# Kernel optimization log

Hardware: AMD Instinct MI355X
Metric: run time of the kernel (lower is better)

## Reference

```python
import jax, jax.numpy as jnp
import numpy as np

B, L, D_MODEL, H = 2, 2048, 1024, 16
D_HEAD = D_MODEL // H
NEG = -1e9


def setup_inputs() -> dict:
    key = jax.random.key(0)
    ks = jax.random.split(key, 8)
    q = jax.random.normal(ks[0], (B, L, D_MODEL), dtype=jnp.float32)
    k = jax.random.normal(ks[1], (B, L, D_MODEL), dtype=jnp.float32)
    v = jax.random.normal(ks[2], (B, L, D_MODEL), dtype=jnp.float32)
    # causal mask: True where attention is disallowed (masked_fill semantics)
    mask = jnp.broadcast_to(jnp.triu(jnp.ones((L, L), dtype=bool), k=1), (B, L, L))
    s = 1.0 / np.sqrt(D_MODEL)
    Wq = jax.random.normal(ks[3], (D_MODEL, D_MODEL), dtype=jnp.float32) * s
    Wk = jax.random.normal(ks[4], (D_MODEL, D_MODEL), dtype=jnp.float32) * s
    Wv = jax.random.normal(ks[5], (D_MODEL, D_MODEL), dtype=jnp.float32) * s
    Wo = jax.random.normal(ks[6], (D_MODEL, D_MODEL), dtype=jnp.float32) * s
    return {"q": q, "k": k, "v": v, "mask": mask,
            "Wq": Wq, "Wk": Wk, "Wv": Wv, "Wo": Wo}


def reference(q, k, v, mask, Wq, Wk, Wv, Wo):
    # projections (Linear, bias=False)
    qh = (q @ Wq).reshape(B, L, H, D_HEAD)
    kh = (k @ Wk).reshape(B, L, H, D_HEAD)
    vh = (v @ Wv).reshape(B, L, H, D_HEAD)
    # per-head scores: contiguous d_model slices == head reshape
    scores = jnp.einsum("bqhd,bkhd->bhqk", qh, kh)
    scores = jnp.where(mask[:, None, :, :], NEG, scores)
    # NOTE: original applies softmax FIRST, then divides by sqrt(d_head)
    weights = jax.nn.softmax(scores, axis=-1) / np.sqrt(D_HEAD).astype(np.float32)
    att = jnp.einsum("bhqk,bkhd->bqhd", weights, vh).reshape(B, L, D_MODEL)
    # dropout is identity in eval mode
    return att @ Wo
```

## Files before the change

kernel.cpp:

```cpp
#include <hip/hip_runtime.h>
#include <hip/hip_bf16.h>

#define BATCH  2
#define SEQ    2048
#define DMODEL 1024
#define NHEAD  16
#define DHEAD  64

typedef _Float16 f16x4 __attribute__((ext_vector_type(4)));
typedef _Float16 f16x8 __attribute__((ext_vector_type(8)));
typedef float    f32x4 __attribute__((ext_vector_type(4)));

union H16 { unsigned short u; _Float16 f; };
__device__ __forceinline__ _Float16 u2h(unsigned short u) { H16 c; c.u = u; return c.f; }
__device__ __forceinline__ unsigned short h2u(_Float16 f) { H16 c; c.f = f; return c.u; }

__device__ __forceinline__ void gll16(const void* g, void* l) {
    __builtin_amdgcn_global_load_lds(
        (const __attribute__((address_space(1))) void*)g,
        (__attribute__((address_space(3))) void*)l, 16, 0, 0);
}

__device__ __forceinline__ float dpp_max16(float x) {
    float t;
    t = __int_as_float(__builtin_amdgcn_update_dpp(0, __float_as_int(x), 0xB1, 0xF, 0xF, true));
    x = fmaxf(x, t);
    t = __int_as_float(__builtin_amdgcn_update_dpp(0, __float_as_int(x), 0x4E, 0xF, 0xF, true));
    x = fmaxf(x, t);
    t = __int_as_float(__builtin_amdgcn_update_dpp(0, __float_as_int(x), 0x124, 0xF, 0xF, true));
    x = fmaxf(x, t);
    t = __int_as_float(__builtin_amdgcn_update_dpp(0, __float_as_int(x), 0x128, 0xF, 0xF, true));
    x = fmaxf(x, t);
    return x;
}

__device__ __forceinline__ void pack_body(const float* __restrict__ W,
                                          _Float16* __restrict__ Phi,
                                          _Float16* __restrict__ Plo)
{
    const int n0 = blockIdx.x * 64;
    const int k0 = blockIdx.y * 64;
    const int t  = threadIdx.x;
    const int nl = t & 63;
    const int kc = (t >> 6) * 16;
    const int n  = n0 + nl;
    const int sw = (n & 3) ^ ((n >> 2) & 3);

    _Float16 hi[16], lo[16];
#pragma unroll
    for (int i = 0; i < 16; i++) {
        float x = W[(size_t)(k0 + kc + i) * DMODEL + n] * 32.0f;
        _Float16 h = (_Float16)x;
        hi[i] = h;
        lo[i] = (_Float16)(x - (float)h);
    }
#pragma unroll
    for (int cc = 0; cc < 2; cc++) {
        const int kk = kc + cc * 8;
        const int g  = kk >> 5;
        const int c  = (kk >> 3) & 3;
        const size_t off = (size_t)n * DMODEL + k0 + g * 32 + ((c ^ sw) << 3);
        *(f16x8*)&Phi[off] = *(f16x8*)&hi[cc * 8];
        if (Plo) *(f16x8*)&Plo[off] = *(f16x8*)&lo[cc * 8];
    }
}

__global__ __launch_bounds__(256) void pack_qkv(const float* __restrict__ Wq,
                                                const float* __restrict__ Wk,
                                                const float* __restrict__ Wv,
                                                _Float16* qhiT, _Float16* qloT,
                                                _Float16* khiT, _Float16* kloT,
                                                _Float16* vhiT)
{
    const int z = blockIdx.z;
    pack_body(z == 0 ? Wq : z == 1 ? Wk : Wv,
              z == 0 ? qhiT : z == 1 ? khiT : vhiT,
              z == 0 ? qloT : z == 1 ? kloT : nullptr);
}

__global__ __launch_bounds__(256) void pack_one(const float* __restrict__ W,
                                                _Float16* Phi)
{
    pack_body(W, Phi, nullptr);
}

template <int SPLIT, int BM, int U, typename CT>
__global__ __launch_bounds__(256) void gemm_mfma(const float* __restrict__ A0,
                                                 const float* __restrict__ A1,
                                                 const _Float16* __restrict__ Bh0,
                                                 const _Float16* __restrict__ Bl0,
                                                 const _Float16* __restrict__ Bh1,
                                                 const _Float16* __restrict__ Bl1,
                                                 CT* __restrict__ C0,
                                                 CT* __restrict__ C1,
                                                 _Float16* __restrict__ Kh,
                                                 _Float16* __restrict__ Kl,
                                                 int N, int K)
{
    constexpr int PBA = BM * 32;
    constexpr int PBB = 128 * 32;
    constexpr int NB  = 2 * U;
    constexpr int AHI = 0;
    constexpr int ALO = NB * PBA;
    constexpr int BHI = (SPLIT == 3 ? 2 : 1) * NB * PBA;
    constexpr int BLO = BHI + NB * PBB;
    constexpr int TOT = BHI + (SPLIT == 3 ? 2 : 1) * NB * PBB;
    constexpr int NT  = (BM == 128) ? 4 : 2;
    __shared__ __align__(16) _Float16 smem[TOT];

    const float*    A  = blockIdx.z ? A1 : A0;
    const _Float16* Bh = blockIdx.z ? Bh1 : Bh0;
    const _Float16* Bl = blockIdx.z ? Bl1 : Bl0;
    CT*             C  = blockIdx.z ? C1 : C0;

    const int m0 = blockIdx.x * BM;
    const int n0 = blockIdx.y * 128;
    const int t    = threadIdx.x;
    const int wave = t >> 6;
    const int lane = t & 63;
    const int quad = lane >> 4;
    const int col  = lane & 15;
    const int wm   = (BM == 128) ? (wave & 1) * 64 : 0;
    const int wn   = (BM == 128) ? (wave >> 1) * 64 : wave * 32;

    const int ar  = (BM == 128) ? (t >> 1) : (t >> 2);
    const int akc = (BM == 128) ? ((t & 1) * 16) : ((t & 3) * 4);
    const int asw = (ar & 3) ^ ((ar >> 2) & 3);
    const float* Ap = A + (size_t)(m0 + ar) * K + akc;

    const _Float16* BhSrc = Bh + (size_t)(n0 + wave * 32 + (lane >> 2)) * K + (lane & 3) * 8;
    const _Float16* BlSrc = (SPLIT == 3)
        ? Bl + (size_t)(n0 + wave * 32 + (lane >> 2)) * K + (lane & 3) * 8 : nullptr;

    const int qe8 = (quad ^ ((col & 3) ^ ((col >> 2) & 3))) * 8;

    f32x4 acc[4][NT];
#pragma unroll
    for (int mt = 0; mt < 4; mt++)
#pragma unroll
        for (int nt = 0; nt < NT; nt++) acc[mt][nt] = (f32x4){0.f, 0.f, 0.f, 0.f};

    float av[16];
    auto loadA = [&](int k0, int sl) {
        if constexpr (BM == 128) {
#pragma unroll
            for (int g = 0; g < 4; g++) {
                float4 x = *(const float4*)(Ap + k0 + g * 4);
                av[g * 4 + 0] = x.x; av[g * 4 + 1] = x.y;
                av[g * 4 + 2] = x.z; av[g * 4 + 3] = x.w;
            }
        } else {
            float4 x = *(const float4*)(Ap + k0);
            float4 y = *(const float4*)(Ap + k0 + 16);
            av[sl * 8 + 0] = x.x; av[sl * 8 + 1] = x.y;
            av[sl * 8 + 2] = x.z; av[sl * 8 + 3] = x.w;
            av[sl * 8 + 4] = y.x; av[sl * 8 + 5] = y.y;
            av[sl * 8 + 6] = y.z; av[sl * 8 + 7] = y.w;
        }
    };
    auto issueB = [&](int k0, int buf) {
        _Float16* d0 = &smem[BHI + buf * PBB + wave * 1024];
        gll16(BhSrc + k0, d0);
        gll16(BhSrc + (size_t)16 * K + k0, d0 + 512);
        if constexpr (SPLIT == 3) {
            _Float16* d1 = &smem[BLO + buf * PBB + wave * 1024];
            gll16(BlSrc + k0, d1);
            gll16(BlSrc + (size_t)16 * K + k0, d1 + 512);
        }
    };
    auto storeA = [&](int sbuf, int sl) {
        if constexpr (BM == 128) {
#pragma unroll
            for (int g = 0; g < 2; g++) {
                f16x8 h, l;
#pragma unroll
                for (int j = 0; j < 8; j++) {
                    float x = av[g * 8 + j];
                    _Float16 hh = (_Float16)x;
                    h[j] = hh;
                    l[j] = (_Float16)(x - (float)hh);
                }
                const int off = ar * 32 + ((((akc >> 3) + g) ^ asw) << 3);
                *(f16x8*)&smem[AHI + sbuf * PBA + off] = h;
                if constexpr (SPLIT == 3)
                    *(f16x8*)&smem[ALO + sbuf * PBA + off] = l;
            }
        } else {
#pragma unroll
            for (int g = 0; g < 2; g++) {
                f16x4 h, l;
#pragma unroll
                for (int j = 0; j < 4; j++) {
                    float x = av[sl * 8 + g * 4 + j];
                    _Float16 hh = (_Float16)x;
                    h[j] = hh;
                    l[j] = (_Float16)(x - (float)hh);
                }
                const int c   = ((akc + g * 16) >> 3);
                const int off = ar * 32 + ((c ^ asw) << 3) + (akc & 4);
                *(f16x4*)&smem[AHI + sbuf * PBA + off] = h;
                if constexpr (SPLIT == 3)
                    *(f16x4*)&smem[ALO + sbuf * PBA + off] = l;
            }
        }
    };
    auto computeStep = [&](int buf) {
        f16x8 ah[4], al[4], bh[NT], bl[NT];
#pragma unroll
        for (int mt = 0; mt < 4; mt++) {
            const int arow = (wm + mt * 16 + col) * 32 + qe8;
            ah[mt] = *(f16x8*)&smem[AHI + buf * PBA + arow];
            if constexpr (SPLIT == 3)
                al[mt] = *(f16x8*)&smem[ALO + buf * PBA + arow];
        }
#pragma unroll
        for (int nt = 0; nt < NT; nt++) {
            const int brow = (wn + nt * 16 + col) * 32 + qe8;
            bh[nt] = *(f16x8*)&smem[BHI + buf * PBB + brow];
            if constexpr (SPLIT == 3)
                bl[nt] = *(f16x8*)&smem[BLO + buf * PBB + brow];
        }
#pragma unroll
        for (int nt = 0; nt < NT; nt++)
#pragma unroll
            for (int mt = 0; mt < 4; mt++) {
                acc[mt][nt] = __builtin_amdgcn_mfma_f32_16x16x32_f16(ah[mt], bh[nt], acc[mt][nt], 0, 0, 0);
                if constexpr (SPLIT == 3) {
                    acc[mt][nt] = __builtin_amdgcn_mfma_f32_16x16x32_f16(ah[mt], bl[nt], acc[mt][nt], 0, 0, 0);
                    acc[mt][nt] = __builtin_amdgcn_mfma_f32_16x16x32_f16(al[mt], bh[nt], acc[mt][nt], 0, 0, 0);
                }
            }
    };

    loadA(0, 0);
    issueB(0, 0);
    storeA(0, 0);
    if constexpr (U == 2) {
        loadA(32, 1);
        issueB(32, 1);
        storeA(1, 1);
    }
    __syncthreads();

    int ph = 0;
    for (int k0 = 0; k0 < K; k0 += 32 * U, ph ^= 1) {
        const int  cb  = ph * U;
        const int  sb  = cb ^ U;
        const bool pre = (k0 + 32 * U < K);
        if (pre) {
            loadA(k0 + 32 * U, 0);
            issueB(k0 + 32 * U, sb);
            if constexpr (U == 2) {
                loadA(k0 + 96, 1);
                issueB(k0 + 96, sb + 1);
            }
        }

        computeStep(cb);
        if constexpr (U == 2) computeStep(cb + 1);

        if (pre) {
            storeA(sb, 0);
            if constexpr (U == 2) storeA(sb + 1, 1);
        }
        __syncthreads();
    }

    const float inv = 1.0f / 32.0f;
#pragma unroll
    for (int mt = 0; mt < 4; mt++)
#pragma unroll
        for (int nt = 0; nt < NT; nt++)
#pragma unroll
            for (int r = 0; r < 4; r++) {
                float val = acc[mt][nt][r] * inv;
                size_t idx = (size_t)(m0 + wm + mt * 16 + quad * 4 + r) * N
                           + n0 + wn + nt * 16 + col;
                if constexpr (SPLIT == 3) {
                    _Float16 h = (_Float16)val;
                    if (blockIdx.z == 0) {
                        _Float16 l = (_Float16)(val - (float)h);
                        C[idx] = (unsigned)h2u(h) | ((unsigned)h2u(l) << 16);
                    } else {
                        Kh[idx] = h;
                        Kl[idx] = (_Float16)(val - (float)h);
                    }
                } else if constexpr (__is_same(CT, _Float16)) {
                    C[idx] = (_Float16)val;
                } else {
                    C[idx] = val;
                }
            }
}

#define AKH 0
#define AKL 8192
#define AVT 16384
#define AVT_SIZE (64 * 72 + 64)
#define AP  (AVT + AVT_SIZE)
#define AP_WAVE (16 * 72)
#define ATOT (AP + 4 * AP_WAVE)

__global__ __launch_bounds__(256) void attn_mfma(unsigned* __restrict__ qa,
                                                 const _Float16* __restrict__ khi,
                                                 const _Float16* __restrict__ klo,
                                                 const _Float16* __restrict__ vh)
{
    __shared__ __align__(16) _Float16 smem[ATOT];

    const int i  = blockIdx.x;
    const int j  = i >> 3;
    const int bh = (i & 7) + ((j & 3) << 3);
    const int qt = (SEQ / 64 - 1) - (j >> 2);
    const int b  = bh >> 4;
    const int h  = bh & 15;
    const int qb = qt * 64;

    const int t    = threadIdx.x;
    const int wave = t >> 6;
    const int lane = t & 63;
    const int quad = lane >> 4;
    const int col  = lane & 15;

    const size_t bbase = (size_t)b * SEQ * DMODEL + (size_t)h * DHEAD;
    const _Float16* vb_ptr = vh + bbase;

    const int qm = qb + wave * 16 + col;
    f16x8 qhi[2], qlo[2];
    {
        const unsigned* qp = qa + bbase + (size_t)qm * DMODEL + quad * 8;
#pragma unroll
        for (int kt = 0; kt < 2; kt++) {
            uint4 u0 = *(const uint4*)(qp + kt * 32);
            uint4 u1 = *(const uint4*)(qp + kt * 32 + 4);
            unsigned us[8] = {u0.x, u0.y, u0.z, u0.w, u1.x, u1.y, u1.z, u1.w};
#pragma unroll
            for (int jj = 0; jj < 8; jj++) {
                qhi[kt][jj] = u2h((unsigned short)(us[jj] & 0xffffu));
                qlo[kt][jj] = u2h((unsigned short)(us[jj] >> 16));
            }
        }
    }

    const int rl0  = wave * 16 + (lane >> 3);
    const int kswz = (lane & 7) ^ ((lane >> 3) & 7);
    const size_t kbase = ((size_t)b * SEQ + rl0) * DMODEL + h * DHEAD + (kswz << 3);

    auto issueK = [&](int kb, int buf) {
        const _Float16* sh = khi + kbase + (size_t)kb * DMODEL;
        const _Float16* sl = klo + kbase + (size_t)kb * DMODEL;
        _Float16* dh = &smem[AKH + buf * 4096 + wave * 1024];
        _Float16* dl = &smem[AKL + buf * 4096 + wave * 1024];
        gll16(sh, dh);
        gll16(sh + (size_t)8 * DMODEL, dh + 512);
        gll16(sl, dl);
        gll16(sl + (size_t)8 * DMODEL, dl + 512);
    };

    const int srow = t >> 2;
    const int sdg  = (t & 3) << 4;
    const int vswz = (t & 3) * 16;
    f16x8 pv[2];
    auto loadV = [&](int kb) {
        const _Float16* vp = vb_ptr + (size_t)(kb + srow) * DMODEL + sdg;
        pv[0] = *(const f16x8*)vp;
        pv[1] = *(const f16x8*)(vp + 8);
    };

    f16x8 kOnes;
#pragma unroll
    for (int jj = 0; jj < 8; jj++) kOnes[jj] = (_Float16)1.0f;

    float m_i[4];
    f32x4 l4 = (f32x4){0.f, 0.f, 0.f, 0.f};
    f32x4 o[4];
#pragma unroll
    for (int r = 0; r < 4; r++) m_i[r] = -1e30f;
#pragma unroll
    for (int dt = 0; dt < 4; dt++) o[dt] = (f32x4){0.f, 0.f, 0.f, 0.f};

    const int wq0 = qb + wave * 16;
    _Float16* Pw = &smem[AP + wave * AP_WAVE];
    const int cs = col & 7;

    loadV(0);
    issueK(0, 0);

    int buf = 0;
    for (int kb = 0; kb <= qb; kb += 64, buf ^= 1) {
        __syncthreads();

#pragma unroll
        for (int jj = 0; jj < 8; jj++) {
            smem[AVT + (sdg + jj    ) * 72 + vswz + srow] = pv[0][jj];
            smem[AVT + (sdg + 8 + jj) * 72 + vswz + srow] = pv[1][jj];
        }
        __syncthreads();

        if (kb + 64 <= qb) { issueK(kb + 64, buf ^ 1); loadV(kb + 64); }

        f32x4 acc[4];
#pragma unroll
        for (int ct = 0; ct < 4; ct++) acc[ct] = (f32x4){0.f, 0.f, 0.f, 0.f};
#pragma unroll
        for (int kt = 0; kt < 2; kt++) {
#pragma unroll
            for (int ct = 0; ct < 4; ct++) {
                const int off = (ct * 16 + col) * 64 + ((((kt << 2) | quad) ^ cs) << 3);
                f16x8 bhi = *(f16x8*)&smem[AKH + buf * 4096 + off];
                f16x8 blo = *(f16x8*)&smem[AKL + buf * 4096 + off];
                acc[ct] = __builtin_amdgcn_mfma_f32_16x16x32_f16(qhi[kt], bhi, acc[ct], 0, 0, 0);
                acc[ct] = __builtin_amdgcn_mfma_f32_16x16x32_f16(qhi[kt], blo, acc[ct], 0, 0, 0);
                acc[ct] = __builtin_amdgcn_mfma_f32_16x16x32_f16(qlo[kt], bhi, acc[ct], 0, 0, 0);
            }
        }

        const bool need_mask = (kb + 63 > wq0);
#pragma unroll
        for (int r = 0; r < 4; r++) {
            const int qrow = wq0 + quad * 4 + r;
            float s0 = acc[0][r], s1 = acc[1][r], s2 = acc[2][r], s3 = acc[3][r];
            if (need_mask) {
                s0 = (kb +  0 + col <= qrow) ? s0 : -1e30f;
                s1 = (kb + 16 + col <= qrow) ? s1 : -1e30f;
                s2 = (kb + 32 + col <= qrow) ? s2 : -1e30f;
                s3 = (kb + 48 + col <= qrow) ? s3 : -1e30f;
            }
            float rm = dpp_max16(fmaxf(fmaxf(s0, s1), fmaxf(s2, s3)));
            const float mnew  = fmaxf(m_i[r], rm);
            const float alpha = __expf(m_i[r] - mnew);
            const float p0 = __expf(s0 - mnew), p1 = __expf(s1 - mnew);
            const float p2 = __expf(s2 - mnew), p3 = __expf(s3 - mnew);
            m_i[r] = mnew;
            l4[r] *= alpha;
#pragma unroll
            for (int dt = 0; dt < 4; dt++) o[dt][r] *= alpha;
            const int prow = quad * 4 + r;
            Pw[prow * 72 + col     ] = (_Float16)p0;
            Pw[prow * 72 + col + 16] = (_Float16)p1;
            Pw[prow * 72 + col + 32] = (_Float16)p2;
            Pw[prow * 72 + col + 48] = (_Float16)p3;
        }

#pragma unroll
        for (int kt = 0; kt < 2; kt++) {
            f16x8 a = *(f16x8*)&Pw[col * 72 + kt * 32 + quad * 8];
            l4 = __builtin_amdgcn_mfma_f32_16x16x32_f16(a, kOnes, l4, 0, 0, 0);
#pragma unroll
            for (int dt = 0; dt < 4; dt++) {
                f16x8 bv = *(f16x8*)&smem[AVT + (dt * 16 + col) * 72 + (dt & 3) * 16 + kt * 32 + quad * 8];
                o[dt] = __builtin_amdgcn_mfma_f32_16x16x32_f16(a, bv, o[dt], 0, 0, 0);
            }
        }
    }

#pragma unroll
    for (int r = 0; r < 4; r++) {
        const float inv = 1.0f / (l4[r] * 8.0f);
        const int q = wq0 + quad * 4 + r;
        unsigned* op = qa + bbase + (size_t)q * DMODEL;
#pragma unroll
        for (int dt = 0; dt < 4; dt++)
            op[dt * 16 + col] = __float_as_uint(o[dt][r] * inv);
    }
}

extern "C" void kernel_launch(void* const* d_in, const int* in_sizes, int n_in,
                              void* d_out, int out_size, void* d_ws, size_t ws_size,
                              hipStream_t stream)
{
    const float* q  = (const float*)d_in[0];
    const float* k  = (const float*)d_in[1];
    const float* v  = (const float*)d_in[2];
    const float* Wq = (const float*)d_in[4];
    const float* Wk = (const float*)d_in[5];
    const float* Wv = (const float*)d_in[6];
    const float* Wo = (const float*)d_in[7];
    float* out = (float*)d_out;

    const int    M   = BATCH * SEQ;
    const size_t npe = (size_t)M * DMODEL;
    const size_t PW  = (size_t)DMODEL * DMODEL;

    unsigned* qh    = (unsigned*)d_ws;
    _Float16* khi_p = (_Float16*)(qh + npe);
    _Float16* klo_p = khi_p + npe;

    _Float16* dh    = (_Float16*)d_out;
    _Float16* qhiT  = dh;
    _Float16* qloT  = dh + PW;
    _Float16* khiT  = dh + 2 * PW;
    _Float16* kloT  = dh + 3 * PW;
    _Float16* vhiT  = dh + 4 * PW;
    _Float16* vh    = dh;
    _Float16* wohiT = khi_p;

    dim3 b256(256);
    dim3 pk(DMODEL / 64, DMODEL / 64, 3);
    dim3 pk1(DMODEL / 64, DMODEL / 64, 1);
    dim3 gqk(M / 128, DMODEL / 128, 2);
    dim3 g64(M / 64, DMODEL / 128, 1);
    dim3 agrid(1024);

    pack_qkv<<<pk, b256, 0, stream>>>(Wq, Wk, Wv, qhiT, qloT, khiT, kloT, vhiT);
    gemm_mfma<3, 128, 1, unsigned><<<gqk, b256, 0, stream>>>(q, k, qhiT, qloT, khiT, kloT,
                                                             qh, nullptr, khi_p, klo_p,
                                                             DMODEL, DMODEL);
    gemm_mfma<1, 64, 2, _Float16><<<g64, b256, 0, stream>>>(v, v, vhiT, nullptr, vhiT, nullptr,
                                                            vh, vh, nullptr, nullptr,
                                                            DMODEL, DMODEL);
    attn_mfma<<<agrid, b256, 0, stream>>>(qh, khi_p, klo_p, vh);
    pack_one<<<pk1, b256, 0, stream>>>(Wo, wohiT);
    gemm_mfma<1, 64, 2, float><<<g64, b256, 0, stream>>>((const float*)qh, (const float*)qh,
                                                         wohiT, nullptr, wohiT, nullptr,
                                                         out, out, nullptr, nullptr,
                                                         DMODEL, DMODEL);
}
```

Baseline: 283.1 us.

## Write V transposed from projection GEMM and stream it into LDS asynchronously

The V projection GEMM now writes its output in a per-head transposed layout (head, d, seq). This lets the attention kernel load V tiles straight into double-buffered, XOR-swizzled LDS with global_load_lds, the same way it loads K. It removes the register staging and the scattered per-element LDS transpose stores, and cuts the barriers per iteration from two to one. The cost is strided, uncoalesced scalar stores in the V GEMM epilogue, which may slow that kernel.

```diff
diff --git a/kernel.cpp b/kernel.cpp
--- a/kernel.cpp
+++ b/kernel.cpp
@@ -84,7 +84,7 @@
     pack_body(W, Phi, nullptr);
 }
 
-template <int SPLIT, int BM, int U, typename CT>
+template <int SPLIT, int BM, int U, typename CT, bool VT = false>
 __global__ __launch_bounds__(256) void gemm_mfma(const float* __restrict__ A0,
                                                  const float* __restrict__ A1,
                                                  const _Float16* __restrict__ Bh0,
@@ -286,7 +286,15 @@
                         Kl[idx] = (_Float16)(val - (float)h);
                     }
                 } else if constexpr (__is_same(CT, _Float16)) {
-                    C[idx] = (_Float16)val;
+                    if constexpr (VT) {
+                        const int mg = m0 + wm + mt * 16 + quad * 4 + r;
+                        const int ng = n0 + wn + nt * 16 + col;
+                        const size_t it = ((size_t)((mg >> 11) * NHEAD + (ng >> 6)) * DHEAD
+                                           + (ng & (DHEAD - 1))) * SEQ + (mg & (SEQ - 1));
+                        C[it] = (_Float16)val;
+                    } else {
+                        C[idx] = (_Float16)val;
+                    }
                 } else {
                     C[idx] = val;
                 }
@@ -296,15 +304,14 @@
 #define AKH 0
 #define AKL 8192
 #define AVT 16384
-#define AVT_SIZE (64 * 72 + 64)
-#define AP  (AVT + AVT_SIZE)
+#define AP  (AVT + 8192)
 #define AP_WAVE (16 * 72)
 #define ATOT (AP + 4 * AP_WAVE)
 
 __global__ __launch_bounds__(256) void attn_mfma(unsigned* __restrict__ qa,
                                                  const _Float16* __restrict__ khi,
                                                  const _Float16* __restrict__ klo,
-                                                 const _Float16* __restrict__ vh)
+                                                 const _Float16* __restrict__ vt)
 {
     __shared__ __align__(16) _Float16 smem[ATOT];
 
@@ -323,7 +330,6 @@
     const int col  = lane & 15;
 
     const size_t bbase = (size_t)b * SEQ * DMODEL + (size_t)h * DHEAD;
-    const _Float16* vb_ptr = vh + bbase;
 
     const int qm = qb + wave * 16 + col;
     f16x8 qhi[2], qlo[2];
@@ -357,14 +363,12 @@
         gll16(sl + (size_t)8 * DMODEL, dl + 512);
     };
 
-    const int srow = t >> 2;
-    const int sdg  = (t & 3) << 4;
-    const int vswz = (t & 3) * 16;
-    f16x8 pv[2];
-    auto loadV = [&](int kb) {
-        const _Float16* vp = vb_ptr + (size_t)(kb + srow) * DMODEL + sdg;
-        pv[0] = *(const f16x8*)vp;
-        pv[1] = *(const f16x8*)(vp + 8);
+    const _Float16* vtb = vt + ((size_t)(b * NHEAD + h) * DHEAD + rl0) * SEQ + (kswz << 3);
+    auto issueV = [&](int kb, int buf) {
+        const _Float16* sv = vtb + kb;
+        _Float16* dv = &smem[AVT + buf * 4096 + wave * 1024];
+        gll16(sv, dv);
+        gll16(sv + (size_t)8 * SEQ, dv + 512);
     };
 
     f16x8 kOnes;
@@ -383,21 +387,16 @@
     _Float16* Pw = &smem[AP + wave * AP_WAVE];
     const int cs = col & 7;
 
-    loadV(0);
     issueK(0, 0);
+    issueV(0, 0);
+    __syncthreads();
 
     int buf = 0;
     for (int kb = 0; kb <= qb; kb += 64, buf ^= 1) {
-        __syncthreads();
-
-#pragma unroll
-        for (int jj = 0; jj < 8; jj++) {
-            smem[AVT + (sdg + jj    ) * 72 + vswz + srow] = pv[0][jj];
-            smem[AVT + (sdg + 8 + jj) * 72 + vswz + srow] = pv[1][jj];
-        }
-        __syncthreads();
-
-        if (kb + 64 <= qb) { issueK(kb + 64, buf ^ 1); loadV(kb + 64); }
+        if (kb + 64 <= qb) {
+            issueK(kb + 64, buf ^ 1);
+            issueV(kb + 64, buf ^ 1);
+        }
 
         f32x4 acc[4];
 #pragma unroll
@@ -448,10 +447,13 @@
             l4 = __builtin_amdgcn_mfma_f32_16x16x32_f16(a, kOnes, l4, 0, 0, 0);
 #pragma unroll
             for (int dt = 0; dt < 4; dt++) {
-                f16x8 bv = *(f16x8*)&smem[AVT + (dt * 16 + col) * 72 + (dt & 3) * 16 + kt * 32 + quad * 8];
+                const int off = (dt * 16 + col) * 64 + ((((kt << 2) | quad) ^ cs) << 3);
+                f16x8 bv = *(f16x8*)&smem[AVT + buf * 4096 + off];
                 o[dt] = __builtin_amdgcn_mfma_f32_16x16x32_f16(a, bv, o[dt], 0, 0, 0);
             }
         }
+
+        __syncthreads();
     }
 
 #pragma unroll
@@ -492,7 +494,7 @@
     _Float16* khiT  = dh + 2 * PW;
     _Float16* kloT  = dh + 3 * PW;
     _Float16* vhiT  = dh + 4 * PW;
-    _Float16* vh    = dh;
+    _Float16* vtp   = dh;
     _Float16* wohiT = khi_p;
 
     dim3 b256(256);
@@ -506,10 +508,10 @@
     gemm_mfma<3, 128, 1, unsigned><<<gqk, b256, 0, stream>>>(q, k, qhiT, qloT, khiT, kloT,
                                                              qh, nullptr, khi_p, klo_p,
                                                              DMODEL, DMODEL);
-    gemm_mfma<1, 64, 2, _Float16><<<g64, b256, 0, stream>>>(v, v, vhiT, nullptr, vhiT, nullptr,
-                                                            vh, vh, nullptr, nullptr,
-                                                            DMODEL, DMODEL);
-    attn_mfma<<<agrid, b256, 0, stream>>>(qh, khi_p, klo_p, vh);
+    gemm_mfma<1, 64, 2, _Float16, true><<<g64, b256, 0, stream>>>(v, v, vhiT, nullptr, vhiT, nullptr,
+                                                                  vtp, vtp, nullptr, nullptr,
+                                                                  DMODEL, DMODEL);
+    attn_mfma<<<agrid, b256, 0, stream>>>(qh, khi_p, klo_p, vtp);
     pack_one<<<pk1, b256, 0, stream>>>(Wo, wohiT);
     gemm_mfma<1, 64, 2, float><<<g64, b256, 0, stream>>>((const float*)qh, (const float*)qh,
                                                          wohiT, nullptr, wohiT, nullptr,
```

Result: slower. 292.2 us (+3.2%).

## Process two 64-row query tiles per attention block to reuse K/V tiles

Applied to the files above, without the earlier changes.

Each attention workgroup now handles 128 query rows as two 64-row sub-tiles (A and B) sharing each staged K/V tile, and the grid is halved to 512 blocks. This halves global K/V loads and LDS staging per query row. The cost is doubled accumulator registers (possible occupancy loss), fewer blocks for load balancing across CUs, and serialization of the two sub-tiles through the same per-wave P buffer.

```diff
diff --git a/kernel.cpp b/kernel.cpp
--- a/kernel.cpp
+++ b/kernel.cpp
@@ -311,10 +311,10 @@
     const int i  = blockIdx.x;
     const int j  = i >> 3;
     const int bh = (i & 7) + ((j & 3) << 3);
-    const int qt = (SEQ / 64 - 1) - (j >> 2);
+    const int qp = (SEQ / 128 - 1) - (j >> 2);
     const int b  = bh >> 4;
     const int h  = bh & 15;
-    const int qb = qt * 64;
+    const int qb = qp * 128;
 
     const int t    = threadIdx.x;
     const int wave = t >> 6;
@@ -325,22 +325,23 @@
     const size_t bbase = (size_t)b * SEQ * DMODEL + (size_t)h * DHEAD;
     const _Float16* vb_ptr = vh + bbase;
 
-    const int qm = qb + wave * 16 + col;
-    f16x8 qhi[2], qlo[2];
-    {
-        const unsigned* qp = qa + bbase + (size_t)qm * DMODEL + quad * 8;
+    f16x8 qhiA[2], qloA[2], qhiB[2], qloB[2];
+    auto loadQ = [&](int qm, f16x8* qh_, f16x8* ql_) {
+        const unsigned* qp_ = qa + bbase + (size_t)qm * DMODEL + quad * 8;
 #pragma unroll
         for (int kt = 0; kt < 2; kt++) {
-            uint4 u0 = *(const uint4*)(qp + kt * 32);
-            uint4 u1 = *(const uint4*)(qp + kt * 32 + 4);
+            uint4 u0 = *(const uint4*)(qp_ + kt * 32);
+            uint4 u1 = *(const uint4*)(qp_ + kt * 32 + 4);
             unsigned us[8] = {u0.x, u0.y, u0.z, u0.w, u1.x, u1.y, u1.z, u1.w};
 #pragma unroll
             for (int jj = 0; jj < 8; jj++) {
-                qhi[kt][jj] = u2h((unsigned short)(us[jj] & 0xffffu));
-                qlo[kt][jj] = u2h((unsigned short)(us[jj] >> 16));
-            }
-        }
-    }
+                qh_[kt][jj] = u2h((unsigned short)(us[jj] & 0xffffu));
+                ql_[kt][jj] = u2h((unsigned short)(us[jj] >> 16));
+            }
+        }
+    };
+    loadQ(qb + wave * 16 + col, qhiA, qloA);
+    loadQ(qb + 64 + wave * 16 + col, qhiB, qloB);
 
     const int rl0  = wave * 16 + (lane >> 3);
     const int kswz = (lane & 7) ^ ((lane >> 3) & 7);
@@ -371,37 +372,24 @@
 #pragma unroll
     for (int jj = 0; jj < 8; jj++) kOnes[jj] = (_Float16)1.0f;
 
-    float m_i[4];
-    f32x4 l4 = (f32x4){0.f, 0.f, 0.f, 0.f};
-    f32x4 o[4];
-#pragma unroll
-    for (int r = 0; r < 4; r++) m_i[r] = -1e30f;
-#pragma unroll
-    for (int dt = 0; dt < 4; dt++) o[dt] = (f32x4){0.f, 0.f, 0.f, 0.f};
-
-    const int wq0 = qb + wave * 16;
+    float mA[4], mB[4];
+    f32x4 lA = (f32x4){0.f, 0.f, 0.f, 0.f};
+    f32x4 lB = (f32x4){0.f, 0.f, 0.f, 0.f};
+    f32x4 oA[4], oB[4];
+#pragma unroll
+    for (int r = 0; r < 4; r++) { mA[r] = -1e30f; mB[r] = -1e30f; }
+#pragma unroll
+    for (int dt = 0; dt < 4; dt++) {
+        oA[dt] = (f32x4){0.f, 0.f, 0.f, 0.f};
+        oB[dt] = (f32x4){0.f, 0.f, 0.f, 0.f};
+    }
+
+    const int wq0A = qb + wave * 16;
+    const int wq0B = wq0A + 64;
     _Float16* Pw = &smem[AP + wave * AP_WAVE];
     const int cs = col & 7;
 
-    loadV(0);
-    issueK(0, 0);
-
-    int buf = 0;
-    for (int kb = 0; kb <= qb; kb += 64, buf ^= 1) {
-        __syncthreads();
-
-#pragma unroll
-        for (int jj = 0; jj < 8; jj++) {
-            smem[AVT + (sdg + jj    ) * 72 + vswz + srow] = pv[0][jj];
-            smem[AVT + (sdg + 8 + jj) * 72 + vswz + srow] = pv[1][jj];
-        }
-        __syncthreads();
-
-        if (kb + 64 <= qb) { issueK(kb + 64, buf ^ 1); loadV(kb + 64); }
-
-        f32x4 acc[4];
-#pragma unroll
-        for (int ct = 0; ct < 4; ct++) acc[ct] = (f32x4){0.f, 0.f, 0.f, 0.f};
+    auto qk3 = [&](f32x4* acc, const f16x8* qh_, const f16x8* ql_, int buf) {
 #pragma unroll
         for (int kt = 0; kt < 2; kt++) {
 #pragma unroll
@@ -409,16 +397,17 @@
                 const int off = (ct * 16 + col) * 64 + ((((kt << 2) | quad) ^ cs) << 3);
                 f16x8 bhi = *(f16x8*)&smem[AKH + buf * 4096 + off];
                 f16x8 blo = *(f16x8*)&smem[AKL + buf * 4096 + off];
-                acc[ct] = __builtin_amdgcn_mfma_f32_16x16x32_f16(qhi[kt], bhi, acc[ct], 0, 0, 0);
-                acc[ct] = __builtin_amdgcn_mfma_f32_16x16x32_f16(qhi[kt], blo, acc[ct], 0, 0, 0);
-                acc[ct] = __builtin_amdgcn_mfma_f32_16x16x32_f16(qlo[kt], bhi, acc[ct], 0, 0, 0);
-            }
-        }
-
-        const bool need_mask = (kb + 63 > wq0);
+                acc[ct] = __builtin_amdgcn_mfma_f32_16x16x32_f16(qh_[kt], bhi, acc[ct], 0, 0, 0);
+                acc[ct] = __builtin_amdgcn_mfma_f32_16x16x32_f16(qh_[kt], blo, acc[ct], 0, 0, 0);
+                acc[ct] = __builtin_amdgcn_mfma_f32_16x16x32_f16(ql_[kt], bhi, acc[ct], 0, 0, 0);
+            }
+        }
+    };
+    auto smx = [&](f32x4* acc, float* mi, f32x4* lv, f32x4* ov, int wq0x, int kb) {
+        const bool need_mask = (kb + 63 > wq0x);
 #pragma unroll
         for (int r = 0; r < 4; r++) {
-            const int qrow = wq0 + quad * 4 + r;
+            const int qrow = wq0x + quad * 4 + r;
             float s0 = acc[0][r], s1 = acc[1][r], s2 = acc[2][r], s3 = acc[3][r];
             if (need_mask) {
                 s0 = (kb +  0 + col <= qrow) ? s0 : -1e30f;
@@ -427,41 +416,82 @@
                 s3 = (kb + 48 + col <= qrow) ? s3 : -1e30f;
             }
             float rm = dpp_max16(fmaxf(fmaxf(s0, s1), fmaxf(s2, s3)));
-            const float mnew  = fmaxf(m_i[r], rm);
-            const float alpha = __expf(m_i[r] - mnew);
+            const float mnew  = fmaxf(mi[r], rm);
+            const float alpha = __expf(mi[r] - mnew);
             const float p0 = __expf(s0 - mnew), p1 = __expf(s1 - mnew);
             const float p2 = __expf(s2 - mnew), p3 = __expf(s3 - mnew);
-            m_i[r] = mnew;
-            l4[r] *= alpha;
-#pragma unroll
-            for (int dt = 0; dt < 4; dt++) o[dt][r] *= alpha;
+            mi[r] = mnew;
+            (*lv)[r] *= alpha;
+#pragma unroll
+            for (int dt = 0; dt < 4; dt++) ov[dt][r] *= alpha;
             const int prow = quad * 4 + r;
             Pw[prow * 72 + col     ] = (_Float16)p0;
             Pw[prow * 72 + col + 16] = (_Float16)p1;
             Pw[prow * 72 + col + 32] = (_Float16)p2;
             Pw[prow * 72 + col + 48] = (_Float16)p3;
         }
-
+    };
+    auto pvf = [&](f32x4* lv, f32x4* ov) {
 #pragma unroll
         for (int kt = 0; kt < 2; kt++) {
             f16x8 a = *(f16x8*)&Pw[col * 72 + kt * 32 + quad * 8];
-            l4 = __builtin_amdgcn_mfma_f32_16x16x32_f16(a, kOnes, l4, 0, 0, 0);
+            *lv = __builtin_amdgcn_mfma_f32_16x16x32_f16(a, kOnes, *lv, 0, 0, 0);
 #pragma unroll
             for (int dt = 0; dt < 4; dt++) {
                 f16x8 bv = *(f16x8*)&smem[AVT + (dt * 16 + col) * 72 + (dt & 3) * 16 + kt * 32 + quad * 8];
-                o[dt] = __builtin_amdgcn_mfma_f32_16x16x32_f16(a, bv, o[dt], 0, 0, 0);
-            }
+                ov[dt] = __builtin_amdgcn_mfma_f32_16x16x32_f16(a, bv, ov[dt], 0, 0, 0);
+            }
+        }
+    };
+
+    loadV(0);
+    issueK(0, 0);
+
+    int buf = 0;
+    for (int kb = 0; kb <= qb + 64; kb += 64, buf ^= 1) {
+        __syncthreads();
+
+#pragma unroll
+        for (int jj = 0; jj < 8; jj++) {
+            smem[AVT + (sdg + jj    ) * 72 + vswz + srow] = pv[0][jj];
+            smem[AVT + (sdg + 8 + jj) * 72 + vswz + srow] = pv[1][jj];
+        }
+        __syncthreads();
+
+        if (kb <= qb) { issueK(kb + 64, buf ^ 1); loadV(kb + 64); }
+
+        if (kb <= qb) {
+            f32x4 acc[4];
+#pragma unroll
+            for (int ct = 0; ct < 4; ct++) acc[ct] = (f32x4){0.f, 0.f, 0.f, 0.f};
+            qk3(acc, qhiA, qloA, buf);
+            smx(acc, mA, &lA, oA, wq0A, kb);
+            pvf(&lA, oA);
+        }
+
+        {
+            f32x4 acc[4];
+#pragma unroll
+            for (int ct = 0; ct < 4; ct++) acc[ct] = (f32x4){0.f, 0.f, 0.f, 0.f};
+            qk3(acc, qhiB, qloB, buf);
+            smx(acc, mB, &lB, oB, wq0B, kb);
+            pvf(&lB, oB);
         }
     }
 
 #pragma unroll
     for (int r = 0; r < 4; r++) {
-        const float inv = 1.0f / (l4[r] * 8.0f);
-        const int q = wq0 + quad * 4 + r;
-        unsigned* op = qa + bbase + (size_t)q * DMODEL;
-#pragma unroll
-        for (int dt = 0; dt < 4; dt++)
-            op[dt * 16 + col] = __float_as_uint(o[dt][r] * inv);
+        const float invA = 1.0f / (lA[r] * 8.0f);
+        const float invB = 1.0f / (lB[r] * 8.0f);
+        const int qA = wq0A + quad * 4 + r;
+        const int qB = wq0B + quad * 4 + r;
+        unsigned* opA = qa + bbase + (size_t)qA * DMODEL;
+        unsigned* opB = qa + bbase + (size_t)qB * DMODEL;
+#pragma unroll
+        for (int dt = 0; dt < 4; dt++) {
+            opA[dt * 16 + col] = __float_as_uint(oA[dt][r] * invA);
+            opB[dt * 16 + col] = __float_as_uint(oB[dt][r] * invB);
+        }
     }
 }
 
@@ -500,7 +530,7 @@
     dim3 pk1(DMODEL / 64, DMODEL / 64, 1);
     dim3 gqk(M / 128, DMODEL / 128, 2);
     dim3 g64(M / 64, DMODEL / 128, 1);
-    dim3 agrid(1024);
+    dim3 agrid(512);
 
     pack_qkv<<<pk, b256, 0, stream>>>(Wq, Wk, Wv, qhiT, qloT, khiT, kloT, vhiT);
     gemm_mfma<3, 128, 1, unsigned><<<gqk, b256, 0, stream>>>(q, k, qhiT, qloT, khiT, kloT,
```

Result: slower. 313.4 us (+10.7%).
